# Performance work log

Measured on AMD Instinct MI355X. Metric: run time of the kernel, lower is better.

## Reference

```python
import jax, jax.numpy as jnp
import numpy as np

N_HEAD = 16
N_EMBD = 1024
HEAD_DIM = N_EMBD // N_HEAD
ROPE_BASE = 10000.0


def _rms_norm(x):
    # F.rms_norm with eps=None uses dtype eps
    eps = jnp.finfo(x.dtype).eps
    ms = jnp.mean(jnp.square(x), axis=-1, keepdims=True)
    return x * jax.lax.rsqrt(ms + eps)


def _rope_tables(T, dtype):
    inv_freq = 1.0 / (ROPE_BASE ** (jnp.arange(0, HEAD_DIM, 2, dtype=jnp.float32) / HEAD_DIM))
    t = jnp.arange(T, dtype=jnp.float32)
    freqs = jnp.outer(t, inv_freq)  # [T, D/2]
    cos = jnp.cos(freqs).astype(dtype)[None, :, None, :]  # [1,T,1,D/2]
    sin = jnp.sin(freqs).astype(dtype)[None, :, None, :]
    return cos, sin


def _apply_rotary(x, cos, sin):
    d = x.shape[-1] // 2
    x1, x2 = x[..., :d], x[..., d:]
    y1 = x1 * cos + x2 * sin
    y2 = -x1 * sin + x2 * cos
    return jnp.concatenate([y1, y2], axis=-1).astype(x.dtype)


def setup_inputs() -> dict:
    key = jax.random.key(0)
    ks = jax.random.split(key, 7)
    B, T, C = 4, 2048, N_EMBD
    s = 0.02
    return {
        "x": jax.random.normal(ks[0], (B, T, C), dtype=jnp.float32),
        "v1": jax.random.normal(ks[1], (B, T, C), dtype=jnp.float32),
        "Wq": jax.random.normal(ks[2], (C, C), dtype=jnp.float32) * s,
        "Wk": jax.random.normal(ks[3], (C, C), dtype=jnp.float32) * s,
        "Wv": jax.random.normal(ks[4], (C, C), dtype=jnp.float32) * s,
        "Wproj": jax.random.normal(ks[5], (C, C), dtype=jnp.float32) * s,
        "lamb": jnp.float32(0.5),
    }


def reference(x, v1, Wq, Wk, Wv, Wproj, lamb):
    B, T, C = x.shape
    H, D = N_HEAD, HEAD_DIM
    q = (x @ Wq.T).reshape(B, T, H, D)
    k = (x @ Wk.T).reshape(B, T, H, D)
    v = (x @ Wv.T).reshape(B, T, H, D)
    # value-lambda residual mix
    v = (1.0 - lamb) * v + lamb * v1.reshape(B, T, H, D)
    # RMSNorm then RoPE on q, k
    cos, sin = _rope_tables(T, x.dtype)
    q = _apply_rotary(_rms_norm(q), cos, sin)
    k = _apply_rotary(_rms_norm(k), cos, sin)
    # causal SDPA
    scale = 1.0 / jnp.sqrt(jnp.float32(D)).astype(x.dtype)
    scores = jnp.einsum("bthd,bshd->bhts", q, k) * scale  # [B,H,T,T]
    causal = jnp.tril(jnp.ones((T, T), dtype=bool))
    scores = jnp.where(causal[None, None], scores, jnp.finfo(scores.dtype).min)
    attn = jax.nn.softmax(scores, axis=-1)
    y = jnp.einsum("bhts,bshd->bthd", attn, v).reshape(B, T, C)
    y = y @ Wproj.T
    return (y, v1)
```

## Files before the change

kernel.cpp:

```cpp
#include <hip/hip_runtime.h>
#include <hip/hip_bf16.h>

typedef __bf16 bf16x8 __attribute__((ext_vector_type(8)));
typedef __bf16 bf16x4 __attribute__((ext_vector_type(4)));
typedef float  f32x4  __attribute__((ext_vector_type(4)));
typedef float  f32x16 __attribute__((ext_vector_type(16)));
typedef unsigned u32x4 __attribute__((ext_vector_type(4)));

#define B_ 4
#define T_ 2048
#define H_ 16
#define D_ 64
#define C_ 1024
#define M_ 8192
#define NE_ ((size_t)M_ * C_)
#define KVSTR_ 2048

__global__ void probe_dtype(const unsigned short* __restrict__ x,
                            int* __restrict__ flag)
{
  __shared__ float red[256];
  float m = 0.0f;
  for (int i = threadIdx.x; i < 4096; i += 256) {
    unsigned int u = ((unsigned int)x[i]) << 16;
    float v = fabsf(__uint_as_float(u));
    if (!(v <= 1e30f)) v = 1e31f;
    m = fmaxf(m, v);
  }
  red[threadIdx.x] = m;
  __syncthreads();
  for (int s = 128; s > 0; s >>= 1) {
    if (threadIdx.x < s) red[threadIdx.x] = fmaxf(red[threadIdx.x], red[threadIdx.x + s]);
    __syncthreads();
  }
  if (threadIdx.x == 0) *flag = (red[0] > 100.0f) ? 1 : 0;
}

__device__ __forceinline__ float load1_adapt(const void* p, size_t idx, int f)
{
  if (f) return ((const float*)p)[idx];
  return __bfloat162float(((const __hip_bfloat16*)p)[idx]);
}

__global__ __launch_bounds__(256) void cvt_bf16(
    const int* __restrict__ flagp, const void* __restrict__ src,
    __bf16* __restrict__ dst, int n)
{
  const int f = *flagp;
  for (size_t i = ((size_t)blockIdx.x * 256 + threadIdx.x) * 8; i < (size_t)n;
       i += (size_t)gridDim.x * 2048) {
    bf16x8 r;
    if (f) {
      const float* pf = (const float*)src + i;
      float4 a = *(const float4*)pf;
      float4 b = *(const float4*)(pf + 4);
      r[0] = (__bf16)a.x; r[1] = (__bf16)a.y; r[2] = (__bf16)a.z; r[3] = (__bf16)a.w;
      r[4] = (__bf16)b.x; r[5] = (__bf16)b.y; r[6] = (__bf16)b.z; r[7] = (__bf16)b.w;
    } else {
      r = *(const bf16x8*)((const __bf16*)src + i);
    }
    *(bf16x8*)(dst + i) = r;
  }
}

__device__ __forceinline__ void g2lds16(const __bf16* g, __bf16* l)
{
  __builtin_amdgcn_global_load_lds(
      (const __attribute__((address_space(1))) void*)g,
      (__attribute__((address_space(3))) void*)l, 16, 0, 0);
}

__device__ __forceinline__ unsigned cvtpk_bf16(float lo, float hi)
{
  unsigned r;
  asm("v_cvt_pk_bf16_f32 %0, %1, %2" : "=v"(r) : "v"(lo), "v"(hi));
  return r;
}

__global__ __launch_bounds__(256) void gemm128(
    const __bf16* __restrict__ A, const __bf16* __restrict__ Bm,
    void* __restrict__ C, int M, int N, int K,
    const int* __restrict__ flagp, int adaptive)
{
  __shared__ __bf16 As[128][64];
  __shared__ __bf16 Bs[128][64];

  const int tid  = threadIdx.x;
  const int wv   = tid >> 6;
  const int lane = tid & 63;
  const int n16  = lane & 15;
  const int quad = lane >> 4;
  const int wm = (wv & 1) * 64, wn = (wv >> 1) * 64;

  const int nwgx = gridDim.x;
  const int id   = blockIdx.y * nwgx + blockIdx.x;
  const int cpx  = (nwgx * gridDim.y) >> 3;
  const int swz  = (id & 7) * cpx + (id >> 3);
  const int m0 = (swz % nwgx) * 128, n0 = (swz / nwgx) * 128;

  f32x4 acc[4][4];
#pragma unroll
  for (int i = 0; i < 4; i++)
#pragma unroll
    for (int j = 0; j < 4; j++) acc[i][j] = (f32x4){0.f, 0.f, 0.f, 0.f};

  const int trow = tid >> 3;
  const int tcol = (tid & 7) * 8;

  for (int k0 = 0; k0 < K; k0 += 64) {
#pragma unroll
    for (int p = 0; p < 4; p++) {
      g2lds16(A  + (size_t)(m0 + trow + p * 32) * K + k0 + tcol,
              &As[trow + p * 32][tcol]);
      g2lds16(Bm + (size_t)(n0 + trow + p * 32) * K + k0 + tcol,
              &Bs[trow + p * 32][tcol]);
    }
    __syncthreads();

#pragma unroll
    for (int kk = 0; kk < 2; kk++) {
      bf16x8 af[4], bf[4];
#pragma unroll
      for (int i = 0; i < 4; i++) {
        af[i] = *(const bf16x8*)&As[wm + i * 16 + n16][kk * 32 + quad * 8];
        bf[i] = *(const bf16x8*)&Bs[wn + i * 16 + n16][kk * 32 + quad * 8];
      }
#pragma unroll
      for (int i = 0; i < 4; i++)
#pragma unroll
        for (int j = 0; j < 4; j++)
          acc[i][j] = __builtin_amdgcn_mfma_f32_16x16x32_bf16(af[i], bf[j],
                                                              acc[i][j], 0, 0, 0);
    }
    __syncthreads();
  }

  const int f = adaptive ? *flagp : 0;
  const int rb = quad * 4;
#pragma unroll
  for (int i = 0; i < 4; i++)
#pragma unroll
    for (int j = 0; j < 4; j++)
#pragma unroll
      for (int r = 0; r < 4; r++) {
        const size_t idx = (size_t)(m0 + wm + i * 16 + rb + r) * N
                           + n0 + wn + j * 16 + n16;
        if (f) ((float*)C)[idx] = acc[i][j][r];
        else   ((__bf16*)C)[idx] = (__bf16)acc[i][j][r];
      }
}

__global__ __launch_bounds__(256) void fuse_rope_vmix(
    const int* __restrict__ flagp,
    __hip_bfloat16* __restrict__ q,
    __hip_bfloat16* __restrict__ kv,
    const void* __restrict__ v1,
    const void* __restrict__ lambp)
{
  const int f    = *flagp;
  const int task = blockIdx.x * 4 + (threadIdx.x >> 6);
  const int lane = threadIdx.x & 63;
  const int h  = task & 15;
  const int bt = task >> 4;
  const int t  = bt & (T_ - 1);
  const size_t baseq = (size_t)bt * C_ + h * D_ + lane;
  const size_t basek = (size_t)bt * KVSTR_ + h * D_ + lane;

  const int j = lane & 31;
  const float inv = expf(-(float)j * (9.2103403719761836f / 32.0f));
  const float ang = (float)t * inv;
  const float cs = cosf(ang), sn = sinf(ang);
  const float EPS = 0.0078125f;

  {
    float xv = __bfloat162float(q[baseq]);
    float ss = xv * xv;
#pragma unroll
    for (int off = 32; off >= 1; off >>= 1) ss += __shfl_xor(ss, off);
    float r  = rsqrtf(ss * (1.0f / 64.0f) + EPS);
    float xn = xv * r;
    float pr = __shfl_xor(xn, 32);
    float yv = (lane < 32) ? (xn * cs + pr * sn) : (pr * -sn + xn * cs);
    q[baseq] = __float2bfloat16(yv);
  }
  {
    float xv = __bfloat162float(kv[basek]);
    float ss = xv * xv;
#pragma unroll
    for (int off = 32; off >= 1; off >>= 1) ss += __shfl_xor(ss, off);
    float r  = rsqrtf(ss * (1.0f / 64.0f) + EPS);
    float xn = xv * r;
    float pr = __shfl_xor(xn, 32);
    float yv = (lane < 32) ? (xn * cs + pr * sn) : (pr * -sn + xn * cs);
    kv[basek] = __float2bfloat16(yv);
  }
  {
    float lam = load1_adapt(lambp, 0, f);
    float vv  = __bfloat162float(kv[basek + 1024]);
    float v1v = load1_adapt(v1, baseq, f);
    kv[basek + 1024] = __float2bfloat16((1.0f - lam) * vv + lam * v1v);
  }
}

__global__ __launch_bounds__(256) void transp_v(
    const __bf16* __restrict__ kv, __bf16* __restrict__ vt)
{
  __shared__ __bf16 Ts[64][72];
  const int bh = blockIdx.y;
  const int t0 = blockIdx.x * 64;
  const int b = bh >> 4, h = bh & 15;

  const int r = threadIdx.x >> 2;
  const int c = (threadIdx.x & 3) * 16;
  const __bf16* src = kv + (size_t)(b * T_ + t0 + r) * KVSTR_ + 1024 + h * D_ + c;
  *(bf16x8*)&Ts[r][c]     = *(const bf16x8*)src;
  *(bf16x8*)&Ts[r][c + 8] = *(const bf16x8*)(src + 8);
  __syncthreads();

  const int d  = threadIdx.x >> 2;
  const int tc = (threadIdx.x & 3) * 16;
  bf16x8 o0, o1;
#pragma unroll
  for (int jj = 0; jj < 8; jj++) { o0[jj] = Ts[tc + jj][d]; o1[jj] = Ts[tc + 8 + jj][d]; }
  __bf16* dst = vt + (size_t)(bh * D_ + d) * T_ + t0 + tc;
  *(bf16x8*)dst       = o0;
  *(bf16x8*)(dst + 8) = o1;
}

__global__ __launch_bounds__(256, 3) void attn_mfma(
    const __bf16* q,
    const __bf16* __restrict__ kv,
    const __bf16* __restrict__ vt,
    __bf16* y)
{
  const int tid  = threadIdx.x;
  const int wv   = tid >> 6;
  const int lane = tid & 63;
  const int l31  = lane & 31;
  const int hi   = lane >> 5;

  const int id = blockIdx.y * gridDim.x + blockIdx.x;
  const int bh = (id & 7) + 8 * ((id >> 3) & 7);
  const int bx = id >> 6;
  const int b = bh >> 4, h = bh & 15;
  const int q0 = (gridDim.x - 1 - bx) * 128;
  const size_t hb  = (size_t)b * T_ * C_ + h * D_;
  const size_t hbk = (size_t)b * T_ * KVSTR_ + h * D_;
  const size_t vhb = (size_t)bh * D_ * T_;

  const int qbase = q0 + wv * 32;

  bf16x8 aq[4];
  {
    const __bf16* qp = q + hb + (size_t)(qbase + l31) * C_ + hi * 8;
#pragma unroll
    for (int i = 0; i < 4; i++) {
      aq[i] = *(const bf16x8*)(qp + 16 * i);
#pragma unroll
      for (int jj = 0; jj < 8; jj++)
        aq[i][jj] = (__bf16)((float)aq[i][jj] * 0.125f);
    }
  }

  f32x16 Ot0, Ot1;
#pragma unroll
  for (int r = 0; r < 16; r++) { Ot0[r] = 0.f; Ot1[r] = 0.f; }
  float l_lane = 0.f;

  const int niter = (qbase + 31) / 64 + 1;
  for (int it = 0; it < niter; it++) {
    const int s0 = it * 64;
    const int nst = (s0 + 32 <= qbase + 31) ? 2 : 1;

    bf16x8 kf[2][4];
#pragma unroll
    for (int st = 0; st < 2; st++) {
      const __bf16* kp = kv + hbk + (size_t)(s0 + 32 * st + l31) * KVSTR_ + hi * 8;
#pragma unroll
      for (int i = 0; i < 4; i++) kf[st][i] = *(const bf16x8*)(kp + 16 * i);
    }
    bf16x8 vf[2][4];
#pragma unroll
    for (int dh = 0; dh < 2; dh++) {
      const __bf16* vp = vt + vhb + (size_t)(32 * dh + l31) * T_ + s0 + hi * 8;
#pragma unroll
      for (int sc = 0; sc < 4; sc++) vf[dh][sc] = *(const bf16x8*)(vp + 16 * sc);
    }

    bf16x8 pf[4];
#pragma unroll
    for (int st = 0; st < 2; st++) {
      if (st < nst) {
        f32x16 S;
#pragma unroll
        for (int r = 0; r < 16; r++) S[r] = 0.f;
        __builtin_amdgcn_s_setprio(1);
#pragma unroll
        for (int i = 0; i < 4; i++)
          S = __builtin_amdgcn_mfma_f32_32x32x16_bf16(kf[st][i], aq[i], S, 0, 0, 0);
        __builtin_amdgcn_s_setprio(0);

        if (s0 + 32 * st + 31 > qbase) {
          const int tg = qbase + l31;
#pragma unroll
          for (int r = 0; r < 16; r++) {
            const int sg = s0 + 32 * st + (r & 3) + 8 * (r >> 2) + 4 * hi;
            if (sg > tg) S[r] = -1e30f;
          }
        }

        float p[16];
#pragma unroll
        for (int r = 0; r < 16; r++) p[r] = __expf(S[r] - 8.0f);
#pragma unroll
        for (int r = 0; r < 16; r++) l_lane += p[r];

        unsigned wg[4][2];
#pragma unroll
        for (int g = 0; g < 4; g++) {
          wg[g][0] = cvtpk_bf16(p[4 * g + 0], p[4 * g + 1]);
          wg[g][1] = cvtpk_bf16(p[4 * g + 2], p[4 * g + 3]);
        }

#pragma unroll
        for (int scl = 0; scl < 2; scl++) {
          unsigned x0 = wg[2 * scl][0], y0 = wg[2 * scl + 1][0];
          unsigned x1 = wg[2 * scl][1], y1 = wg[2 * scl + 1][1];
          asm volatile("v_permlane32_swap_b32 %0, %1" : "+v"(x0), "+v"(y0));
          asm volatile("v_permlane32_swap_b32 %0, %1" : "+v"(x1), "+v"(y1));
          union { u32x4 u; bf16x8 v8; } uw;
          uw.u[0] = x0; uw.u[1] = x1; uw.u[2] = y0; uw.u[3] = y1;
          pf[2 * st + scl] = uw.v8;
        }
      }
    }

    const int nsc = 2 * nst;
    __builtin_amdgcn_s_setprio(1);
#pragma unroll
    for (int sc = 0; sc < 4; sc++)
      if (sc < nsc) {
        Ot0 = __builtin_amdgcn_mfma_f32_32x32x16_bf16(vf[0][sc], pf[sc], Ot0, 0, 0, 0);
        Ot1 = __builtin_amdgcn_mfma_f32_32x32x16_bf16(vf[1][sc], pf[sc], Ot1, 0, 0, 0);
      }
    __builtin_amdgcn_s_setprio(0);
  }

  l_lane += __shfl_xor(l_lane, 32);
  const float linv = 1.0f / l_lane;
  const int qrow = qbase + l31;
#pragma unroll
  for (int g = 0; g < 4; g++) {
    bf16x4 o0, o1;
#pragma unroll
    for (int m = 0; m < 4; m++) {
      o0[m] = (__bf16)(Ot0[4 * g + m] * linv);
      o1[m] = (__bf16)(Ot1[4 * g + m] * linv);
    }
    const int d0 = 8 * g + 4 * hi;
    *(bf16x4*)(y + hb + (size_t)qrow * C_ + d0)      = o0;
    *(bf16x4*)(y + hb + (size_t)qrow * C_ + 32 + d0) = o1;
  }
}

__global__ __launch_bounds__(256) void copy_v1(
    const int* __restrict__ flagp, const void* __restrict__ v1, void* __restrict__ out)
{
  const int f = *flagp;
  const size_t nbytes = NE_ * (f ? 4u : 2u);
  const uint4* s = (const uint4*)v1;
  uint4* d = (uint4*)((char*)out + nbytes);
  const size_t n16 = nbytes / 16;
  for (size_t i = (size_t)blockIdx.x * 256 + threadIdx.x; i < n16;
       i += (size_t)gridDim.x * 256)
    d[i] = s[i];
}

extern "C" void kernel_launch(void* const* d_in, const int* in_sizes, int n_in,
                              void* d_out, int out_size, void* d_ws, size_t ws_size,
                              hipStream_t stream)
{
  const void* x    = d_in[0];
  const void* v1   = d_in[1];
  const void* Wq   = d_in[2];
  const void* Wk   = d_in[3];
  const void* Wv   = d_in[4];
  const void* Wp   = d_in[5];
  const void* lamb = d_in[6];

  __bf16* xb  = (__bf16*)d_ws;
  __bf16* qw  = xb + NE_;
  __bf16* wqb = qw + NE_;
  __bf16* wkb = wqb + (size_t)C_ * C_;
  __bf16* wvb = wkb + (size_t)C_ * C_;
  __bf16* wpb = wvb + (size_t)C_ * C_;
  int* flagp  = (int*)(wpb + (size_t)C_ * C_);
  __bf16* vtb = xb;
  __bf16* kvw = (__bf16*)d_out;

  probe_dtype<<<1, 256, 0, stream>>>((const unsigned short*)x, flagp);

  cvt_bf16<<<4096, 256, 0, stream>>>(flagp, x,  xb,  (int)NE_);
  cvt_bf16<<<512,  256, 0, stream>>>(flagp, Wq, wqb, C_ * C_);
  cvt_bf16<<<512,  256, 0, stream>>>(flagp, Wk, wkb, C_ * C_);
  cvt_bf16<<<512,  256, 0, stream>>>(flagp, Wv, wvb, C_ * C_);
  cvt_bf16<<<512,  256, 0, stream>>>(flagp, Wp, wpb, C_ * C_);

  gemm128<<<dim3(M_ / 128, 8),  256, 0, stream>>>(xb, wqb, qw,  M_, 1024, C_, flagp, 0);
  gemm128<<<dim3(M_ / 128, 16), 256, 0, stream>>>(xb, wkb, kvw, M_, 2048, C_, flagp, 0);

  fuse_rope_vmix<<<(M_ * H_) / 4, 256, 0, stream>>>(
      flagp, (__hip_bfloat16*)qw, (__hip_bfloat16*)kvw, v1, lamb);

  transp_v<<<dim3(T_ / 64, B_ * H_), 256, 0, stream>>>(kvw, vtb);

  attn_mfma<<<dim3(T_ / 128, B_ * H_), 256, 0, stream>>>(qw, kvw, vtb, qw);

  gemm128<<<dim3(M_ / 128, 8), 256, 0, stream>>>(qw, wpb, d_out, M_, 1024, C_, flagp, 1);
  copy_v1<<<8192, 256, 0, stream>>>(flagp, v1, d_out);
}
```

Measured before the change: 444.0 us.

## Pre-pack K and V into MFMA fragment order for coalesced attention loads

```diff
diff --git a/kernel.cpp b/kernel.cpp
--- a/kernel.cpp
+++ b/kernel.cpp
@@ -203,11 +203,12 @@
 }
 
 __global__ __launch_bounds__(256) void transp_v(
-    const __bf16* __restrict__ kv, __bf16* __restrict__ vt)
+    const __bf16* __restrict__ kv, __bf16* __restrict__ pvt)
 {
   __shared__ __bf16 Ts[64][72];
   const int bh = blockIdx.y;
-  const int t0 = blockIdx.x * 64;
+  const int it = blockIdx.x;
+  const int t0 = it * 64;
   const int b = bh >> 4, h = bh & 15;
 
   const int r = threadIdx.x >> 2;
@@ -218,19 +219,39 @@
   __syncthreads();
 
   const int d  = threadIdx.x >> 2;
-  const int tc = (threadIdx.x & 3) * 16;
+  const int sc = threadIdx.x & 3;
   bf16x8 o0, o1;
 #pragma unroll
-  for (int jj = 0; jj < 8; jj++) { o0[jj] = Ts[tc + jj][d]; o1[jj] = Ts[tc + 8 + jj][d]; }
-  __bf16* dst = vt + (size_t)(bh * D_ + d) * T_ + t0 + tc;
-  *(bf16x8*)dst       = o0;
-  *(bf16x8*)(dst + 8) = o1;
+  for (int jj = 0; jj < 8; jj++) {
+    o0[jj] = Ts[sc * 16 + jj][d];
+    o1[jj] = Ts[sc * 16 + 8 + jj][d];
+  }
+  const int dh = d >> 5, l31 = d & 31;
+  __bf16* dst = pvt + (((size_t)bh * 32 + it) * 2 + dh) * 2048 + sc * 512 + l31 * 8;
+  *(bf16x8*)dst         = o0;
+  *(bf16x8*)(dst + 256) = o1;
+}
+
+__global__ __launch_bounds__(256) void pack_k(__bf16* kv)
+{
+  const int cid = blockIdx.x * 256 + threadIdx.x;
+  const int lane = cid & 63;
+  const int i    = (cid >> 6) & 3;
+  const int st   = (cid >> 8) & 1;
+  const int it   = (cid >> 9) & 31;
+  const int bh   = cid >> 14;
+  const int b = bh >> 4, h = bh & 15;
+  const int l31 = lane & 31, hi = lane >> 5;
+  const int t = 64 * it + 32 * st + l31;
+  const int d = 16 * i + 8 * hi;
+  bf16x8 v = *(const bf16x8*)(kv + (size_t)(b * T_ + t) * KVSTR_ + h * D_ + d);
+  *(bf16x8*)(kv + (size_t)(cid >> 7) * KVSTR_ + 1024 + (cid & 127) * 8) = v;
 }
 
 __global__ __launch_bounds__(256, 3) void attn_mfma(
     const __bf16* q,
-    const __bf16* __restrict__ kv,
-    const __bf16* __restrict__ vt,
+    const __bf16* __restrict__ pk,
+    const __bf16* __restrict__ pvt,
     __bf16* y)
 {
   const int tid  = threadIdx.x;
@@ -240,13 +261,11 @@
   const int hi   = lane >> 5;
 
   const int id = blockIdx.y * gridDim.x + blockIdx.x;
-  const int bh = (id & 7) + 8 * ((id >> 3) & 7);
+  const int bh = id & 63;
   const int bx = id >> 6;
   const int b = bh >> 4, h = bh & 15;
   const int q0 = (gridDim.x - 1 - bx) * 128;
-  const size_t hb  = (size_t)b * T_ * C_ + h * D_;
-  const size_t hbk = (size_t)b * T_ * KVSTR_ + h * D_;
-  const size_t vhb = (size_t)bh * D_ * T_;
+  const size_t hb = (size_t)b * T_ * C_ + h * D_;
 
   const int qbase = q0 + wv * 32;
 
@@ -272,20 +291,21 @@
     const int s0 = it * 64;
     const int nst = (s0 + 32 <= qbase + 31) ? 2 : 1;
 
-    bf16x8 kf[2][4];
-#pragma unroll
-    for (int st = 0; st < 2; st++) {
-      const __bf16* kp = kv + hbk + (size_t)(s0 + 32 * st + l31) * KVSTR_ + hi * 8;
-#pragma unroll
-      for (int i = 0; i < 4; i++) kf[st][i] = *(const bf16x8*)(kp + 16 * i);
-    }
-    bf16x8 vf[2][4];
-#pragma unroll
-    for (int dh = 0; dh < 2; dh++) {
-      const __bf16* vp = vt + vhb + (size_t)(32 * dh + l31) * T_ + s0 + hi * 8;
-#pragma unroll
-      for (int sc = 0; sc < 4; sc++) vf[dh][sc] = *(const bf16x8*)(vp + 16 * sc);
-    }
+    const __bf16* pkb = pk  + (((size_t)bh * 32 + it) * 4) * KVSTR_ + 1024 + lane * 8;
+    const __bf16* pvb = pvt + (((size_t)bh * 32 + it) * 2) * 2048 + lane * 8;
+    bf16x8 kf[2][4], vf[2][4];
+#pragma unroll
+    for (int st = 0; st < 2; st++)
+#pragma unroll
+      for (int i = 0; i < 4; i++) {
+        const int f = st * 4 + i;
+        kf[st][i] = *(const bf16x8*)(pkb + (f >> 1) * KVSTR_ + (f & 1) * 512);
+      }
+#pragma unroll
+    for (int dh = 0; dh < 2; dh++)
+#pragma unroll
+      for (int sc = 0; sc < 4; sc++)
+        vf[dh][sc] = *(const bf16x8*)(pvb + dh * 2048 + sc * 512);
 
     bf16x8 pf[4];
 #pragma unroll
@@ -395,7 +415,7 @@
   __bf16* wvb = wkb + (size_t)C_ * C_;
   __bf16* wpb = wvb + (size_t)C_ * C_;
   int* flagp  = (int*)(wpb + (size_t)C_ * C_);
-  __bf16* vtb = xb;
+  __bf16* pvtb = xb;
   __bf16* kvw = (__bf16*)d_out;
 
   probe_dtype<<<1, 256, 0, stream>>>((const unsigned short*)x, flagp);
@@ -412,9 +432,10 @@
   fuse_rope_vmix<<<(M_ * H_) / 4, 256, 0, stream>>>(
       flagp, (__hip_bfloat16*)qw, (__hip_bfloat16*)kvw, v1, lamb);
 
-  transp_v<<<dim3(T_ / 64, B_ * H_), 256, 0, stream>>>(kvw, vtb);
-
-  attn_mfma<<<dim3(T_ / 128, B_ * H_), 256, 0, stream>>>(qw, kvw, vtb, qw);
+  transp_v<<<dim3(T_ / 64, B_ * H_), 256, 0, stream>>>(kvw, pvtb);
+  pack_k<<<4096, 256, 0, stream>>>(kvw);
+
+  attn_mfma<<<dim3(T_ / 128, B_ * H_), 256, 0, stream>>>(qw, kvw, pvtb, qw);
 
   gemm128<<<dim3(M_ / 128, 8), 256, 0, stream>>>(qw, wpb, d_out, M_, 1024, C_, flagp, 1);
   copy_v1<<<8192, 256, 0, stream>>>(flagp, v1, d_out);
```

Measured after the change: 378.2 us. 14.8% less time.
